# Optimization experiments

Hardware: AMD Instinct MI355X
Metric: run time of the kernel (lower is better)

## Reference

```python
import jax, jax.numpy as jnp
import numpy as np

N_NODES = 50000
N_EDGES = 300000
N_CLUSTERS = 100
IN_C = 256
OUT_C = 256


def setup_inputs() -> dict:
    key = jax.random.key(0)
    k1, k2, k3, k4, k5, k6 = jax.random.split(key, 6)
    X = jax.random.normal(k1, (N_NODES, IN_C), dtype=jnp.float32)
    # Cluster-GCN style block partition: contiguous clusters of equal size
    assign = ((jnp.arange(N_NODES) * N_CLUSTERS) // N_NODES).astype(jnp.int32)
    bs = N_NODES // N_CLUSTERS  # block (cluster) size
    src = jax.random.randint(k2, (N_EDGES,), 0, N_NODES)
    intra_dst = (src // bs) * bs + jax.random.randint(k3, (N_EDGES,), 0, bs)
    rand_dst = jax.random.randint(k4, (N_EDGES,), 0, N_NODES)
    dst = jnp.where(jax.random.uniform(k5, (N_EDGES,)) < 0.9, intra_dst, rand_dst)
    full_ei = jnp.stack([src, dst]).astype(jnp.int32)
    W = (jax.random.normal(k6, (IN_C, OUT_C), dtype=jnp.float32) / np.sqrt(IN_C)).astype(jnp.float32)
    b = jnp.zeros((OUT_C,), dtype=jnp.float32)
    return {"X": X, "W": W, "b": b, "assign": assign, "full_ei": full_ei}


def reference(X, W, b, assign, full_ei):
    # Equivalent to the per-cluster loop: GCNConv (add_self_loops=True, symmetric
    # normalization) applied to the subgraph of intra-cluster edges; clusters
    # with zero internal edges are skipped (nodes keep original features).
    N = X.shape[0]
    src, dst = full_ei[0], full_ei[1]
    intra = (assign[src] == assign[dst]).astype(X.dtype)  # [E]
    # per-cluster-subgraph degree, including self loop
    deg = jnp.ones((N,), X.dtype).at[dst].add(intra)  # [N]
    dis = jax.lax.rsqrt(deg)
    xW = X @ W  # [N, out_c]
    w_e = intra * dis[src] * dis[dst]  # [E]
    agg = jax.ops.segment_sum(w_e[:, None] * xW[src], dst, num_segments=N)
    agg = agg + xW / deg[:, None]  # self-loop term: norm = 1/deg
    out = agg + b
    has_edge = jax.ops.segment_sum(intra, assign[src], num_segments=N_CLUSTERS) > 0
    return jnp.where(has_edge[assign][:, None], out, X)
```

## Files before the change

kernel.cpp:

```cpp
#include <hip/hip_runtime.h>
#include <hip/hip_bf16.h>

#define N_NODES 50000
#define N_EDGES 300000
#define N_CLUSTERS 100
#define CH 256
#define CAP 32

typedef __attribute__((ext_vector_type(8))) short short8;
typedef __attribute__((ext_vector_type(4))) float f32x4;

static __device__ inline unsigned short f2bf(float f) {
    unsigned int u = __float_as_uint(f);
    u += 0x7fffu + ((u >> 16) & 1u);
    return (unsigned short)(u >> 16);
}


__global__ void init_kernel(int* __restrict__ indeg, int* __restrict__ flags) {
    int i = blockIdx.x * blockDim.x + threadIdx.x;
    if (i < N_NODES) indeg[i] = 0;
    if (i < N_CLUSTERS) flags[i] = 0;
}

__global__ void scatter_kernel(const int* __restrict__ ei, const int* __restrict__ assign,
                               int* __restrict__ indeg, int* __restrict__ flags,
                               int* __restrict__ csr) {
    int e = blockIdx.x * blockDim.x + threadIdx.x;
    if (e >= N_EDGES) return;
    int s = ei[e], d = ei[N_EDGES + e];
    int cs = assign[s];
    if (cs == assign[d]) {
        int p = atomicAdd(&indeg[d], 1);
        if (p < CAP) csr[d * CAP + p] = s;
        flags[cs] = 1;
    }
}

__global__ void dis_kernel(const int* __restrict__ indeg, float* __restrict__ dis) {
    int i = blockIdx.x * blockDim.x + threadIdx.x;
    if (i < N_NODES) dis[i] = rsqrtf(1.0f + (float)indeg[i]);
}


__global__ void convx_kernel(const float* __restrict__ X, unsigned short* __restrict__ Xb) {
    int i = blockIdx.x * blockDim.x + threadIdx.x;
    size_t base = (size_t)i * 8;
    if (base >= (size_t)N_NODES * CH) return;
    const float4* xp = reinterpret_cast<const float4*>(X + base);
    float4 a = xp[0], b = xp[1];
    ushort4 lo = { f2bf(a.x), f2bf(a.y), f2bf(a.z), f2bf(a.w) };
    ushort4 hi = { f2bf(b.x), f2bf(b.y), f2bf(b.z), f2bf(b.w) };
    *reinterpret_cast<ushort4*>(Xb + base)     = lo;
    *reinterpret_cast<ushort4*>(Xb + base + 4) = hi;
}

__global__ void convw_kernel(const float* __restrict__ W, unsigned short* __restrict__ Wt) {
    int n = blockIdx.x, k = threadIdx.x;
    Wt[n * CH + k] = f2bf(W[k * CH + n]);
}


#define BM 128
#define BN 128
#define BK 32
#define LDSS 40

__global__ __launch_bounds__(256) void gemm_bf16(const unsigned short* __restrict__ Xb,
                                                 const unsigned short* __restrict__ Wt,
                                                 unsigned short* __restrict__ xWb) {
    __shared__ unsigned short Xs[BM * LDSS];
    __shared__ unsigned short Ws[BN * LDSS];
    int tid = threadIdx.x;
    int bn = blockIdx.x & 1;
    int bm = blockIdx.x >> 1;
    int row0 = bm * BM, col0 = bn * BN;
    int wid = tid >> 6, lane = tid & 63;
    int wm = (wid & 1) * 64, wn = (wid >> 1) * 64;
    int l15 = lane & 15, quad = lane >> 4;

    f32x4 acc[4][4] = {};

    int srow = tid >> 1;
    int skc  = (tid & 1) * 16;
    int garow = row0 + srow; if (garow >= N_NODES) garow = N_NODES - 1;
    const unsigned short* gA = Xb + (size_t)garow * CH + skc;
    const unsigned short* gB = Wt + (size_t)(col0 + srow) * CH + skc;
    unsigned short* lA = &Xs[srow * LDSS + skc];
    unsigned short* lB = &Ws[srow * LDSS + skc];

    for (int k0 = 0; k0 < CH; k0 += BK) {
        uint4 a0 = *reinterpret_cast<const uint4*>(gA + k0);
        uint4 a1 = *reinterpret_cast<const uint4*>(gA + k0 + 8);
        uint4 b0 = *reinterpret_cast<const uint4*>(gB + k0);
        uint4 b1 = *reinterpret_cast<const uint4*>(gB + k0 + 8);
        *reinterpret_cast<uint4*>(lA)     = a0;
        *reinterpret_cast<uint4*>(lA + 8) = a1;
        *reinterpret_cast<uint4*>(lB)     = b0;
        *reinterpret_cast<uint4*>(lB + 8) = b1;
        __syncthreads();

        short8 af[4], bf[4];
#pragma unroll
        for (int mi = 0; mi < 4; ++mi)
            af[mi] = *reinterpret_cast<const short8*>(&Xs[(wm + mi * 16 + l15) * LDSS + quad * 8]);
#pragma unroll
        for (int ni = 0; ni < 4; ++ni)
            bf[ni] = *reinterpret_cast<const short8*>(&Ws[(wn + ni * 16 + l15) * LDSS + quad * 8]);
#pragma unroll
        for (int mi = 0; mi < 4; ++mi)
#pragma unroll
            for (int ni = 0; ni < 4; ++ni)
                acc[mi][ni] = __builtin_amdgcn_mfma_f32_16x16x32_bf16(af[mi], bf[ni], acc[mi][ni], 0, 0, 0);
        __syncthreads();
    }

#pragma unroll
    for (int mi = 0; mi < 4; ++mi) {
#pragma unroll
        for (int r = 0; r < 4; ++r) {
            int grow = row0 + wm + mi * 16 + quad * 4 + r;
            if (grow < N_NODES) {
                size_t rb = (size_t)grow * CH + col0 + wn + l15;
#pragma unroll
                for (int ni = 0; ni < 4; ++ni)
                    xWb[rb + ni * 16] = f2bf(acc[mi][ni][r]);
            }
        }
    }
}


__global__ __launch_bounds__(256) void gather_kernel(const unsigned short* __restrict__ xWb,
        const float* __restrict__ X, const float* __restrict__ b,
        const int* __restrict__ assign, const int* __restrict__ flags,
        const int* __restrict__ indeg, const float* __restrict__ dis,
        const int* __restrict__ csr, float* __restrict__ out) {
    int node = blockIdx.x * 4 + (threadIdx.x >> 6);
    int lane = threadIdx.x & 63;
    if (node >= N_NODES) return;
    float4* out4 = reinterpret_cast<float4*>(out);
    size_t base4 = (size_t)node * 64 + lane;
    if (flags[assign[node]] == 0) {
        out4[base4] = reinterpret_cast<const float4*>(X)[base4];
        return;
    }
    float dn = dis[node];
    float selfw = dn * dn;
    uint2 sv = *reinterpret_cast<const uint2*>(xWb + (size_t)node * CH + lane * 4);
    float ax = selfw * __uint_as_float(sv.x << 16);
    float ay = selfw * __uint_as_float(sv.x & 0xffff0000u);
    float az = selfw * __uint_as_float(sv.y << 16);
    float aw = selfw * __uint_as_float(sv.y & 0xffff0000u);
    int cnt = indeg[node]; if (cnt > CAP) cnt = CAP;
    const int* mycsr = csr + node * CAP;
    for (int i = 0; i < cnt; ++i) {
        int s = mycsr[i];
        float w = dis[s] * dn;
        uint2 v = *reinterpret_cast<const uint2*>(xWb + (size_t)s * CH + lane * 4);
        ax += w * __uint_as_float(v.x << 16);
        ay += w * __uint_as_float(v.x & 0xffff0000u);
        az += w * __uint_as_float(v.y << 16);
        aw += w * __uint_as_float(v.y & 0xffff0000u);
    }
    float4 bb = reinterpret_cast<const float4*>(b)[lane];
    float4 o = { ax + bb.x, ay + bb.y, az + bb.z, aw + bb.w };
    out4[base4] = o;
}


extern "C" void kernel_launch(void* const* d_in, const int* in_sizes, int n_in,
                              void* d_out, int out_size, void* d_ws, size_t ws_size,
                              hipStream_t stream) {
    const float* X      = (const float*)d_in[0];
    const float* W      = (const float*)d_in[1];
    const float* b      = (const float*)d_in[2];
    const int*   assign = (const int*)d_in[3];
    const int*   ei     = (const int*)d_in[4];
    float* out = (float*)d_out;

    char* ws = (char*)d_ws;
    size_t off = 0;
    auto alloc = [&](size_t bytes) -> void* {
        void* p = ws + off;
        off = (off + bytes + 255) & ~(size_t)255;
        return p;
    };
    unsigned short* Xb  = (unsigned short*)alloc((size_t)N_NODES * CH * sizeof(unsigned short));
    unsigned short* xWb = (unsigned short*)alloc((size_t)N_NODES * CH * sizeof(unsigned short));
    unsigned short* Wt  = (unsigned short*)alloc((size_t)CH * CH * sizeof(unsigned short));
    int*   csr   = (int*)alloc((size_t)N_NODES * CAP * sizeof(int));
    int*   indeg = (int*)alloc(N_NODES * sizeof(int));
    float* dis   = (float*)alloc(N_NODES * sizeof(float));
    int*   flags = (int*)alloc(N_CLUSTERS * sizeof(int));
    (void)ws_size; (void)n_in; (void)in_sizes; (void)out_size;

    init_kernel<<<(N_NODES + 255) / 256, 256, 0, stream>>>(indeg, flags);
    scatter_kernel<<<(N_EDGES + 255) / 256, 256, 0, stream>>>(ei, assign, indeg, flags, csr);
    dis_kernel<<<(N_NODES + 255) / 256, 256, 0, stream>>>(indeg, dis);
    convx_kernel<<<((N_NODES * CH / 8) + 255) / 256, 256, 0, stream>>>(X, Xb);
    convw_kernel<<<CH, CH, 0, stream>>>(W, Wt);
    gemm_bf16<<<((N_NODES + BM - 1) / BM) * 2, 256, 0, stream>>>(Xb, Wt, xWb);
    gather_kernel<<<(N_NODES + 3) / 4, 256, 0, stream>>>(xWb, X, b, assign, flags, indeg,
                                                         dis, csr, out);
}
```

Baseline: 201.1 us.

## Fuse X bf16 conversion into GEMM loads and batch gather neighbor loads

```diff
diff --git a/kernel.cpp b/kernel.cpp
--- a/kernel.cpp
+++ b/kernel.cpp
@@ -42,19 +42,6 @@
     if (i < N_NODES) dis[i] = rsqrtf(1.0f + (float)indeg[i]);
 }
 
-
-__global__ void convx_kernel(const float* __restrict__ X, unsigned short* __restrict__ Xb) {
-    int i = blockIdx.x * blockDim.x + threadIdx.x;
-    size_t base = (size_t)i * 8;
-    if (base >= (size_t)N_NODES * CH) return;
-    const float4* xp = reinterpret_cast<const float4*>(X + base);
-    float4 a = xp[0], b = xp[1];
-    ushort4 lo = { f2bf(a.x), f2bf(a.y), f2bf(a.z), f2bf(a.w) };
-    ushort4 hi = { f2bf(b.x), f2bf(b.y), f2bf(b.z), f2bf(b.w) };
-    *reinterpret_cast<ushort4*>(Xb + base)     = lo;
-    *reinterpret_cast<ushort4*>(Xb + base + 4) = hi;
-}
-
 __global__ void convw_kernel(const float* __restrict__ W, unsigned short* __restrict__ Wt) {
     int n = blockIdx.x, k = threadIdx.x;
     Wt[n * CH + k] = f2bf(W[k * CH + n]);
@@ -66,7 +53,7 @@
 #define BK 32
 #define LDSS 40
 
-__global__ __launch_bounds__(256) void gemm_bf16(const unsigned short* __restrict__ Xb,
+__global__ __launch_bounds__(256) void gemm_bf16(const float* __restrict__ X,
                                                  const unsigned short* __restrict__ Wt,
                                                  unsigned short* __restrict__ xWb) {
     __shared__ unsigned short Xs[BM * LDSS];
@@ -84,18 +71,26 @@
     int srow = tid >> 1;
     int skc  = (tid & 1) * 16;
     int garow = row0 + srow; if (garow >= N_NODES) garow = N_NODES - 1;
-    const unsigned short* gA = Xb + (size_t)garow * CH + skc;
+    const float*          gA = X  + (size_t)garow * CH + skc;
     const unsigned short* gB = Wt + (size_t)(col0 + srow) * CH + skc;
     unsigned short* lA = &Xs[srow * LDSS + skc];
     unsigned short* lB = &Ws[srow * LDSS + skc];
 
     for (int k0 = 0; k0 < CH; k0 += BK) {
-        uint4 a0 = *reinterpret_cast<const uint4*>(gA + k0);
-        uint4 a1 = *reinterpret_cast<const uint4*>(gA + k0 + 8);
+        float4 x0 = *reinterpret_cast<const float4*>(gA + k0);
+        float4 x1 = *reinterpret_cast<const float4*>(gA + k0 + 4);
+        float4 x2 = *reinterpret_cast<const float4*>(gA + k0 + 8);
+        float4 x3 = *reinterpret_cast<const float4*>(gA + k0 + 12);
         uint4 b0 = *reinterpret_cast<const uint4*>(gB + k0);
         uint4 b1 = *reinterpret_cast<const uint4*>(gB + k0 + 8);
-        *reinterpret_cast<uint4*>(lA)     = a0;
-        *reinterpret_cast<uint4*>(lA + 8) = a1;
+        ushort4 a0 = { f2bf(x0.x), f2bf(x0.y), f2bf(x0.z), f2bf(x0.w) };
+        ushort4 a1 = { f2bf(x1.x), f2bf(x1.y), f2bf(x1.z), f2bf(x1.w) };
+        ushort4 a2 = { f2bf(x2.x), f2bf(x2.y), f2bf(x2.z), f2bf(x2.w) };
+        ushort4 a3 = { f2bf(x3.x), f2bf(x3.y), f2bf(x3.z), f2bf(x3.w) };
+        *reinterpret_cast<ushort4*>(lA)      = a0;
+        *reinterpret_cast<ushort4*>(lA + 4)  = a1;
+        *reinterpret_cast<ushort4*>(lA + 8)  = a2;
+        *reinterpret_cast<ushort4*>(lA + 12) = a3;
         *reinterpret_cast<uint4*>(lB)     = b0;
         *reinterpret_cast<uint4*>(lB + 8) = b1;
         __syncthreads();
@@ -130,6 +125,13 @@
     }
 }
 
+
+static __device__ inline void bf4_fma(float w, uint2 v, float& ax, float& ay, float& az, float& aw) {
+    ax += w * __uint_as_float(v.x << 16);
+    ay += w * __uint_as_float(v.x & 0xffff0000u);
+    az += w * __uint_as_float(v.y << 16);
+    aw += w * __uint_as_float(v.y & 0xffff0000u);
+}
 
 __global__ __launch_bounds__(256) void gather_kernel(const unsigned short* __restrict__ xWb,
         const float* __restrict__ X, const float* __restrict__ b,
@@ -146,23 +148,42 @@
         return;
     }
     float dn = dis[node];
+    int cnt = indeg[node]; if (cnt > CAP) cnt = CAP;
+
+    int   s_l = 0;
+    float w_l = 0.0f;
+    if (lane < cnt) {
+        s_l = csr[node * CAP + lane];
+        w_l = dis[s_l] * dn;
+    }
+
     float selfw = dn * dn;
     uint2 sv = *reinterpret_cast<const uint2*>(xWb + (size_t)node * CH + lane * 4);
-    float ax = selfw * __uint_as_float(sv.x << 16);
-    float ay = selfw * __uint_as_float(sv.x & 0xffff0000u);
-    float az = selfw * __uint_as_float(sv.y << 16);
-    float aw = selfw * __uint_as_float(sv.y & 0xffff0000u);
-    int cnt = indeg[node]; if (cnt > CAP) cnt = CAP;
-    const int* mycsr = csr + node * CAP;
-    for (int i = 0; i < cnt; ++i) {
-        int s = mycsr[i];
-        float w = dis[s] * dn;
+    float ax = 0, ay = 0, az = 0, aw = 0;
+    bf4_fma(selfw, sv, ax, ay, az, aw);
+
+    int i = 0;
+    for (; i + 4 <= cnt; i += 4) {
+        int   s0 = __shfl(s_l, i),     s1 = __shfl(s_l, i + 1);
+        int   s2 = __shfl(s_l, i + 2), s3 = __shfl(s_l, i + 3);
+        float w0 = __shfl(w_l, i),     w1 = __shfl(w_l, i + 1);
+        float w2 = __shfl(w_l, i + 2), w3 = __shfl(w_l, i + 3);
+        uint2 v0 = *reinterpret_cast<const uint2*>(xWb + (size_t)s0 * CH + lane * 4);
+        uint2 v1 = *reinterpret_cast<const uint2*>(xWb + (size_t)s1 * CH + lane * 4);
+        uint2 v2 = *reinterpret_cast<const uint2*>(xWb + (size_t)s2 * CH + lane * 4);
+        uint2 v3 = *reinterpret_cast<const uint2*>(xWb + (size_t)s3 * CH + lane * 4);
+        bf4_fma(w0, v0, ax, ay, az, aw);
+        bf4_fma(w1, v1, ax, ay, az, aw);
+        bf4_fma(w2, v2, ax, ay, az, aw);
+        bf4_fma(w3, v3, ax, ay, az, aw);
+    }
+    for (; i < cnt; ++i) {
+        int   s = __shfl(s_l, i);
+        float w = __shfl(w_l, i);
         uint2 v = *reinterpret_cast<const uint2*>(xWb + (size_t)s * CH + lane * 4);
-        ax += w * __uint_as_float(v.x << 16);
-        ay += w * __uint_as_float(v.x & 0xffff0000u);
-        az += w * __uint_as_float(v.y << 16);
-        aw += w * __uint_as_float(v.y & 0xffff0000u);
-    }
+        bf4_fma(w, v, ax, ay, az, aw);
+    }
+
     float4 bb = reinterpret_cast<const float4*>(b)[lane];
     float4 o = { ax + bb.x, ay + bb.y, az + bb.z, aw + bb.w };
     out4[base4] = o;
@@ -186,7 +207,6 @@
         off = (off + bytes + 255) & ~(size_t)255;
         return p;
     };
-    unsigned short* Xb  = (unsigned short*)alloc((size_t)N_NODES * CH * sizeof(unsigned short));
     unsigned short* xWb = (unsigned short*)alloc((size_t)N_NODES * CH * sizeof(unsigned short));
     unsigned short* Wt  = (unsigned short*)alloc((size_t)CH * CH * sizeof(unsigned short));
     int*   csr   = (int*)alloc((size_t)N_NODES * CAP * sizeof(int));
@@ -198,9 +218,8 @@
     init_kernel<<<(N_NODES + 255) / 256, 256, 0, stream>>>(indeg, flags);
     scatter_kernel<<<(N_EDGES + 255) / 256, 256, 0, stream>>>(ei, assign, indeg, flags, csr);
     dis_kernel<<<(N_NODES + 255) / 256, 256, 0, stream>>>(indeg, dis);
-    convx_kernel<<<((N_NODES * CH / 8) + 255) / 256, 256, 0, stream>>>(X, Xb);
     convw_kernel<<<CH, CH, 0, stream>>>(W, Wt);
-    gemm_bf16<<<((N_NODES + BM - 1) / BM) * 2, 256, 0, stream>>>(Xb, Wt, xWb);
+    gemm_bf16<<<((N_NODES + BM - 1) / BM) * 2, 256, 0, stream>>>(X, Wt, xWb);
     gather_kernel<<<(N_NODES + 3) / 4, 256, 0, stream>>>(xWb, X, b, assign, flags, indeg,
                                                          dis, csr, out);
 }
```

Result: faster. 175.5 us (-12.7%).
